# Performance work log

Measured on AMD Instinct MI355X. Metric: run time of the kernel, lower is better.

The kernel has to match this reference:

```python
import jax, jax.numpy as jnp
import numpy as np

INPUT_DIM = 28
OUTPUT_DIM = 21
LAYER_SIZE = 64
NUM_HIDDEN = 10  # number of 64x64 hidden layers after the input layer


def setup_inputs() -> dict:
    key = jax.random.key(0)
    ks = jax.random.split(key, 7)
    x = jax.random.normal(ks[0], (1048576, INPUT_DIM), dtype=jnp.float32)
    # PyTorch nn.Linear default init: U(-1/sqrt(fan_in), 1/sqrt(fan_in)); plain uniform is fine for a baseline.
    s_in = 1.0 / np.sqrt(INPUT_DIM)
    s_h = 1.0 / np.sqrt(LAYER_SIZE)
    W_in = jax.random.uniform(ks[1], (INPUT_DIM, LAYER_SIZE), jnp.float32, -s_in, s_in)
    b_in = jax.random.uniform(ks[2], (LAYER_SIZE,), jnp.float32, -s_in, s_in)
    W_hid = jax.random.uniform(ks[3], (NUM_HIDDEN, LAYER_SIZE, LAYER_SIZE), jnp.float32, -s_h, s_h)
    b_hid = jax.random.uniform(ks[4], (NUM_HIDDEN, LAYER_SIZE), jnp.float32, -s_h, s_h)
    W_out = jax.random.uniform(ks[5], (LAYER_SIZE, OUTPUT_DIM), jnp.float32, -s_h, s_h)
    b_out = jax.random.uniform(ks[6], (OUTPUT_DIM,), jnp.float32, -s_h, s_h)
    return {"x": x, "W_in": W_in, "b_in": b_in, "W_hid": W_hid, "b_hid": b_hid,
            "W_out": W_out, "b_out": b_out}


def reference(x, W_in, b_in, W_hid, b_hid, W_out, b_out):
    h = jax.nn.relu(x @ W_in + b_in)  # [B, 64]
    def step(h, wb):
        W, b = wb
        return jax.nn.relu(h @ W + b), None
    h, _ = jax.lax.scan(step, h, (W_hid, b_hid))
    return jax.nn.sigmoid(h @ W_out + b_out)  # [B, 21]
```

## Files before the change

### kernel.cpp

```cpp
#include <hip/hip_runtime.h>

#define DEV __device__ __forceinline__
#define SBAR() __builtin_amdgcn_sched_barrier(0)

typedef _Float16 half8 __attribute__((ext_vector_type(8)));
typedef _Float16 half2v __attribute__((ext_vector_type(2)));
typedef float f32x16 __attribute__((ext_vector_type(16)));
typedef int int4v __attribute__((ext_vector_type(4)));

DEV f32x16 mfma16(half8 a, half8 b, f32x16 c) {
    return __builtin_amdgcn_mfma_f32_32x32x16_f16(a, b, c, 0, 0, 0);
}
DEV half8 h8(int4v v) { return __builtin_bit_cast(half8, v); }
DEV half8 ldh8(const _Float16* p) { return *(const half8*)p; }
DEV int pkrtz(float a, float b) {
    auto t = __builtin_amdgcn_cvt_pkrtz(a, b);
    return __builtin_bit_cast(int, t);
}
DEV int relupk(float a, float b) {
    int p = pkrtz(a, b);
    half2v h = __builtin_bit_cast(half2v, p);
    half2v z = {(_Float16)0.f, (_Float16)0.f};
    h = __builtin_elementwise_max(h, z);
    return __builtin_bit_cast(int, h);
}
DEV void plswap(int& a, int& b) {
    asm("v_permlane32_swap_b32 %0, %1" : "+v"(a), "+v"(b));
}

DEV f32x16 zero16() {
    f32x16 z = {0.f,0.f,0.f,0.f,0.f,0.f,0.f,0.f,0.f,0.f,0.f,0.f,0.f,0.f,0.f,0.f};
    return z;
}

struct Frags { int4v c[4]; };

DEV void repack(const f32x16& C0, const f32x16& C1, Frags& B) {
    int P0[8], P1[8];
#pragma unroll
    for (int q = 0; q < 8; ++q) {
        P0[q] = relupk(C0[2*q], C0[2*q+1]);
        P1[q] = relupk(C1[2*q], C1[2*q+1]);
    }
#pragma unroll
    for (int kk = 0; kk < 4; ++kk) {
        const int* Pm = (kk < 2) ? P0 : P1;
        int idx = 4 * (kk & 1);
        int a0 = Pm[idx + 0], b0 = Pm[idx + 2];
        int a1 = Pm[idx + 1], b1 = Pm[idx + 3];
        plswap(a0, b0);
        plswap(a1, b1);
        int4v nb; nb[0] = a0; nb[1] = a1; nb[2] = b0; nb[3] = b1;
        B.c[kk] = nb;
    }
}

DEV void loadA5(const _Float16* base, int lam, half8* A0, half8* A1) {
    const _Float16* p0 = base + lam * 8;
    const _Float16* p1 = base + 2560 + lam * 8;
#pragma unroll
    for (int kk = 0; kk < 5; ++kk) {
        A0[kk] = ldh8(p0 + kk * 512);
        A1[kk] = ldh8(p1 + kk * 512);
    }
}

DEV void mfma_hid_t(const half8* A0, const half8* A1, half8 ones, const Frags& Bx,
                    f32x16& C0, f32x16& C1) {
    C0 = mfma16(A0[4], ones, zero16());
    C1 = mfma16(A1[4], ones, zero16());
#pragma unroll
    for (int kk = 0; kk < 4; ++kk) {
        half8 b = h8(Bx.c[kk]);
        C0 = mfma16(A0[kk], b, C0);
        C1 = mfma16(A1[kk], b, C1);
    }
}

DEV void mfma_in_t(const half8* I, const Frags& Bx, f32x16& C0, f32x16& C1) {
    C0 = mfma16(I[0], h8(Bx.c[0]), zero16());
    C1 = mfma16(I[2], h8(Bx.c[0]), zero16());
    C0 = mfma16(I[1], h8(Bx.c[1]), C0);
    C1 = mfma16(I[3], h8(Bx.c[1]), C1);
}

DEV void mfma_out_t(const half8* Ao, half8 ones, const Frags& Bx, f32x16& C) {
    C = mfma16(Ao[4], ones, zero16());
#pragma unroll
    for (int kk = 0; kk < 4; ++kk) C = mfma16(Ao[kk], h8(Bx.c[kk]), C);
}

DEV void store_out(const f32x16& C, int h, float* __restrict__ out, int row) {
    float* o = out + row * 21;
#pragma unroll
    for (int r = 0; r < 16; ++r) {
        int f = (r & 3) + 8 * (r >> 2) + 4 * h;
        if (f < 21) o[f] = __builtin_amdgcn_rcpf(1.f + __expf(-C[r]));
    }
}

DEV void load_x(const float* __restrict__ x, int row, int h, Frags& B) {
    const float* xr = x + row * 28;
    float4 fa = *(const float4*)(xr + 8 * h);
    float4 fb = *(const float4*)(xr + 8 * h + 4);
    float4 fc = *(const float4*)(xr + 16 + 8 * h);
    float4 fd = (h == 0) ? *(const float4*)(xr + 20) : make_float4(1.f, 0.f, 0.f, 0.f);
    int4v c0, c1;
    c0[0] = pkrtz(fa.x, fa.y); c0[1] = pkrtz(fa.z, fa.w);
    c0[2] = pkrtz(fb.x, fb.y); c0[3] = pkrtz(fb.z, fb.w);
    c1[0] = pkrtz(fc.x, fc.y); c1[1] = pkrtz(fc.z, fc.w);
    c1[2] = pkrtz(fd.x, fd.y); c1[3] = pkrtz(fd.z, fd.w);
    B.c[0] = c0; B.c[1] = c1;
}

#define NT 512

__global__ __attribute__((amdgpu_flat_work_group_size(NT, NT), amdgpu_waves_per_eu(2, 2)))
void mlp_fused(
    const float* __restrict__ x, const float* __restrict__ W_in, const float* __restrict__ b_in,
    const float* __restrict__ W_hid, const float* __restrict__ b_hid,
    const float* __restrict__ W_out, const float* __restrict__ b_out,
    float* __restrict__ out) {
    __shared__ __align__(16) _Float16 wH[51200];
    __shared__ __align__(16) _Float16 wI[2048];
    __shared__ __align__(16) _Float16 wO[2560];

    const int tid = threadIdx.x;

    for (int i = tid; i < 10240; i += NT) {
        int l = i >> 10, rem = i & 1023, m = rem >> 9, off = rem & 511;
        wH[l * 5120 + m * 2560 + 2048 + off] = (_Float16)0.f;
    }
    for (int i = tid; i < 2048; i += NT) wI[i] = (_Float16)0.f;
    for (int i = tid; i < 2560; i += NT) wO[i] = (_Float16)0.f;
    __syncthreads();

    for (int i = tid; i < 40960; i += NT) {
        int o = i & 63, kin = (i >> 6) & 63, l = i >> 12;
        int m = o >> 5, kk = kin >> 4, hh = (kin >> 3) & 1, e = kin & 7;
        int lam = hh * 32 + (o & 31);
        wH[l * 5120 + m * 2560 + kk * 512 + lam * 8 + e] = (_Float16)W_hid[i];
    }
    for (int i = tid; i < 640; i += NT) {
        int l = i >> 6, f = i & 63, m = f >> 5, r = f & 31;
        wH[l * 5120 + m * 2560 + 2048 + r * 8] = (_Float16)b_hid[i];
    }
    for (int i = tid; i < 1792; i += NT) {
        int o = i & 63, kin = i >> 6;
        int m = o >> 5, kk = kin >> 4, hh = (kin >> 3) & 1, e = kin & 7;
        int lam = hh * 32 + (o & 31);
        wI[m * 1024 + kk * 512 + lam * 8 + e] = (_Float16)W_in[i];
    }
    for (int i = tid; i < 64; i += NT) {
        int m = i >> 5;
        wI[m * 1024 + 512 + (32 + (i & 31)) * 8 + 4] = (_Float16)b_in[i];
    }
    for (int i = tid; i < 1344; i += NT) {
        int o = i % 21, kin = i / 21;
        int kk = kin >> 4, hh = (kin >> 3) & 1, e = kin & 7;
        int lam = hh * 32 + o;
        wO[kk * 512 + lam * 8 + e] = (_Float16)W_out[i];
    }
    for (int i = tid; i < 21; i += NT)
        wO[4 * 512 + i * 8] = (_Float16)b_out[i];
    __syncthreads();

    const int w = tid >> 6, lam = tid & 63;
    const int col = lam & 31, h = lam >> 5;
    int4v onesv; onesv[0] = (h == 0) ? 0x3C00 : 0; onesv[1] = 0; onesv[2] = 0; onesv[3] = 0;
    half8 ones = h8(onesv);

    half8 I[4], Ao[5];
    {
        const _Float16* p0 = wI + lam * 8;
        const _Float16* p1 = wI + 1024 + lam * 8;
        I[0] = ldh8(p0);       I[1] = ldh8(p0 + 512);
        I[2] = ldh8(p1);       I[3] = ldh8(p1 + 512);
        const _Float16* po = wO + lam * 8;
#pragma unroll
        for (int kk = 0; kk < 5; ++kk) Ao[kk] = ldh8(po + kk * 512);
    }

    const int tbase = blockIdx.x * 128;
#pragma unroll 1
    for (int j = 0; j < 8; ++j) {
        int tA = tbase + w * 16 + 2 * j;
        int rowA = tA * 32 + col, rowB = rowA + 32;
        Frags BA, BB;
        load_x(x, rowA, h, BA);
        load_x(x, rowB, h, BB);

        half8 Fa0[5], Fa1[5], Fb0[5], Fb1[5];
        f32x16 CA0, CA1, CB0, CB1;

        mfma_in_t(I, BA, CA0, CA1);
        loadA5(wH, lam, Fa0, Fa1);
        mfma_in_t(I, BB, CB0, CB1);
        repack(CA0, CA1, BA);
        SBAR();

#pragma unroll
        for (int l2 = 0; l2 < 5; ++l2) {
            const _Float16* b0 = wH + (2 * l2) * 5120;
            mfma_hid_t(Fa0, Fa1, ones, BA, CA0, CA1);
            loadA5(b0 + 5120, lam, Fb0, Fb1);
            repack(CB0, CB1, BB);
            SBAR();
            mfma_hid_t(Fa0, Fa1, ones, BB, CB0, CB1);
            repack(CA0, CA1, BA);
            SBAR();
            mfma_hid_t(Fb0, Fb1, ones, BA, CA0, CA1);
            if (l2 < 4) loadA5(b0 + 10240, lam, Fa0, Fa1);
            repack(CB0, CB1, BB);
            SBAR();
            mfma_hid_t(Fb0, Fb1, ones, BB, CB0, CB1);
            repack(CA0, CA1, BA);
            SBAR();
        }

        f32x16 CoA, CoB;
        mfma_out_t(Ao, ones, BA, CoA);
        repack(CB0, CB1, BB);
        SBAR();
        mfma_out_t(Ao, ones, BB, CoB);
        store_out(CoA, h, out, rowA);
        store_out(CoB, h, out, rowB);
    }
}

extern "C" void kernel_launch(void* const* d_in, const int* in_sizes, int n_in,
                              void* d_out, int out_size, void* d_ws, size_t ws_size,
                              hipStream_t stream) {
    const float* x     = (const float*)d_in[0];
    const float* W_in  = (const float*)d_in[1];
    const float* b_in  = (const float*)d_in[2];
    const float* W_hid = (const float*)d_in[3];
    const float* b_hid = (const float*)d_in[4];
    const float* W_out = (const float*)d_in[5];
    const float* b_out = (const float*)d_in[6];
    float* out = (float*)d_out;
    mlp_fused<<<dim3(256), dim3(NT), 0, stream>>>(x, W_in, b_in, W_hid, b_hid, W_out, b_out, out);
}
```

Baseline: 105.9 us.

## Batch both row tiles' MFMAs per layer and raise priority around MFMA bursts

Replaces the staggered ping-pong schedule, in which tile A's MFMAs overlapped tile B's repack, with a schedule that runs both tiles' MFMAs back-to-back for each layer and then repacks both. Interleaving independent A and B accumulators gives the matrix unit more independent chains. It also wraps each MFMA burst in s_setprio so this wave's matrix work gets issue priority over the other waves' VALU repack phases. The cost is that the intra-wave overlap of repack with MFMA is lost, and the design relies on cross-wave overlap, with two waves per EU, to hide the repack instead.

After: 102.2 us. -3.5%, faster.

```diff
diff --git a/kernel.cpp b/kernel.cpp
--- a/kernel.cpp
+++ b/kernel.cpp
@@ -65,29 +65,45 @@
     }
 }
 
-DEV void mfma_hid_t(const half8* A0, const half8* A1, half8 ones, const Frags& Bx,
-                    f32x16& C0, f32x16& C1) {
-    C0 = mfma16(A0[4], ones, zero16());
-    C1 = mfma16(A1[4], ones, zero16());
+DEV void mfma_hid_AB(const half8* A0, const half8* A1, half8 ones,
+                     const Frags& BA, const Frags& BB,
+                     f32x16& CA0, f32x16& CA1, f32x16& CB0, f32x16& CB1) {
+    CA0 = mfma16(A0[4], ones, zero16());
+    CB0 = mfma16(A0[4], ones, zero16());
+    CA1 = mfma16(A1[4], ones, zero16());
+    CB1 = mfma16(A1[4], ones, zero16());
 #pragma unroll
     for (int kk = 0; kk < 4; ++kk) {
-        half8 b = h8(Bx.c[kk]);
-        C0 = mfma16(A0[kk], b, C0);
-        C1 = mfma16(A1[kk], b, C1);
-    }
-}
-
-DEV void mfma_in_t(const half8* I, const Frags& Bx, f32x16& C0, f32x16& C1) {
-    C0 = mfma16(I[0], h8(Bx.c[0]), zero16());
-    C1 = mfma16(I[2], h8(Bx.c[0]), zero16());
-    C0 = mfma16(I[1], h8(Bx.c[1]), C0);
-    C1 = mfma16(I[3], h8(Bx.c[1]), C1);
-}
-
-DEV void mfma_out_t(const half8* Ao, half8 ones, const Frags& Bx, f32x16& C) {
-    C = mfma16(Ao[4], ones, zero16());
-#pragma unroll
-    for (int kk = 0; kk < 4; ++kk) C = mfma16(Ao[kk], h8(Bx.c[kk]), C);
+        half8 bA = h8(BA.c[kk]);
+        half8 bB = h8(BB.c[kk]);
+        CA0 = mfma16(A0[kk], bA, CA0);
+        CB0 = mfma16(A0[kk], bB, CB0);
+        CA1 = mfma16(A1[kk], bA, CA1);
+        CB1 = mfma16(A1[kk], bB, CB1);
+    }
+}
+
+DEV void mfma_in_AB(const half8* I, const Frags& BA, const Frags& BB,
+                    f32x16& CA0, f32x16& CA1, f32x16& CB0, f32x16& CB1) {
+    CA0 = mfma16(I[0], h8(BA.c[0]), zero16());
+    CB0 = mfma16(I[0], h8(BB.c[0]), zero16());
+    CA1 = mfma16(I[2], h8(BA.c[0]), zero16());
+    CB1 = mfma16(I[2], h8(BB.c[0]), zero16());
+    CA0 = mfma16(I[1], h8(BA.c[1]), CA0);
+    CB0 = mfma16(I[1], h8(BB.c[1]), CB0);
+    CA1 = mfma16(I[3], h8(BA.c[1]), CA1);
+    CB1 = mfma16(I[3], h8(BB.c[1]), CB1);
+}
+
+DEV void mfma_out_AB(const half8* Ao, half8 ones, const Frags& BA, const Frags& BB,
+                     f32x16& CoA, f32x16& CoB) {
+    CoA = mfma16(Ao[4], ones, zero16());
+    CoB = mfma16(Ao[4], ones, zero16());
+#pragma unroll
+    for (int kk = 0; kk < 4; ++kk) {
+        CoA = mfma16(Ao[kk], h8(BA.c[kk]), CoA);
+        CoB = mfma16(Ao[kk], h8(BB.c[kk]), CoB);
+    }
 }
 
 DEV void store_out(const f32x16& C, int h, float* __restrict__ out, int row) {
@@ -193,36 +209,37 @@
         half8 Fa0[5], Fa1[5], Fb0[5], Fb1[5];
         f32x16 CA0, CA1, CB0, CB1;
 
-        mfma_in_t(I, BA, CA0, CA1);
+        __builtin_amdgcn_s_setprio(1);
+        mfma_in_AB(I, BA, BB, CA0, CA1, CB0, CB1);
+        __builtin_amdgcn_s_setprio(0);
         loadA5(wH, lam, Fa0, Fa1);
-        mfma_in_t(I, BB, CB0, CB1);
         repack(CA0, CA1, BA);
+        repack(CB0, CB1, BB);
         SBAR();
 
 #pragma unroll
         for (int l2 = 0; l2 < 5; ++l2) {
             const _Float16* b0 = wH + (2 * l2) * 5120;
-            mfma_hid_t(Fa0, Fa1, ones, BA, CA0, CA1);
+            __builtin_amdgcn_s_setprio(1);
+            mfma_hid_AB(Fa0, Fa1, ones, BA, BB, CA0, CA1, CB0, CB1);
+            __builtin_amdgcn_s_setprio(0);
             loadA5(b0 + 5120, lam, Fb0, Fb1);
+            repack(CA0, CA1, BA);
             repack(CB0, CB1, BB);
             SBAR();
-            mfma_hid_t(Fa0, Fa1, ones, BB, CB0, CB1);
+            __builtin_amdgcn_s_setprio(1);
+            mfma_hid_AB(Fb0, Fb1, ones, BA, BB, CA0, CA1, CB0, CB1);
+            __builtin_amdgcn_s_setprio(0);
+            if (l2 < 4) loadA5(b0 + 10240, lam, Fa0, Fa1);
             repack(CA0, CA1, BA);
-            SBAR();
-            mfma_hid_t(Fb0, Fb1, ones, BA, CA0, CA1);
-            if (l2 < 4) loadA5(b0 + 10240, lam, Fa0, Fa1);
             repack(CB0, CB1, BB);
             SBAR();
-            mfma_hid_t(Fb0, Fb1, ones, BB, CB0, CB1);
-            repack(CA0, CA1, BA);
-            SBAR();
         }
 
         f32x16 CoA, CoB;
-        mfma_out_t(Ao, ones, BA, CoA);
-        repack(CB0, CB1, BB);
-        SBAR();
-        mfma_out_t(Ao, ones, BB, CoB);
+        __builtin_amdgcn_s_setprio(1);
+        mfma_out_AB(Ao, ones, BA, BB, CoA, CoB);
+        __builtin_amdgcn_s_setprio(0);
         store_out(CoA, h, out, rowA);
         store_out(CoB, h, out, rowB);
     }
```

## Permute weight K-layout to drop permlane swaps in activation repack

Applied to the files above, without the earlier changes.

Rearranges the K ordering of hidden and output weights in shared memory so the MFMA accumulator layout maps directly onto the next layer's B-operand fragments. This removes the v_permlane32_swap instructions from repack, leaving only relu+pack conversions. It also removes the explicit sched_barrier calls, giving the compiler freedom to interleave repack with MFMAs. The input-layer weights keep the old layout, which is fine only if the K permutation is consistent between the producing and consuming layers. Scheduling freedom may or may not reproduce the hand-tuned interleave.

New measurement: 271.4 us. 156% more time.

```diff
diff --git a/kernel.cpp b/kernel.cpp
--- a/kernel.cpp
+++ b/kernel.cpp
@@ -1,7 +1,6 @@
 #include <hip/hip_runtime.h>
 
 #define DEV __device__ __forceinline__
-#define SBAR() __builtin_amdgcn_sched_barrier(0)
 
 typedef _Float16 half8 __attribute__((ext_vector_type(8)));
 typedef _Float16 half2v __attribute__((ext_vector_type(2)));
@@ -24,9 +23,6 @@
     h = __builtin_elementwise_max(h, z);
     return __builtin_bit_cast(int, h);
 }
-DEV void plswap(int& a, int& b) {
-    asm("v_permlane32_swap_b32 %0, %1" : "+v"(a), "+v"(b));
-}
 
 DEV f32x16 zero16() {
     f32x16 z = {0.f,0.f,0.f,0.f,0.f,0.f,0.f,0.f,0.f,0.f,0.f,0.f,0.f,0.f,0.f,0.f};
@@ -36,23 +32,15 @@
 struct Frags { int4v c[4]; };
 
 DEV void repack(const f32x16& C0, const f32x16& C1, Frags& B) {
-    int P0[8], P1[8];
-#pragma unroll
-    for (int q = 0; q < 8; ++q) {
-        P0[q] = relupk(C0[2*q], C0[2*q+1]);
-        P1[q] = relupk(C1[2*q], C1[2*q+1]);
-    }
-#pragma unroll
-    for (int kk = 0; kk < 4; ++kk) {
-        const int* Pm = (kk < 2) ? P0 : P1;
-        int idx = 4 * (kk & 1);
-        int a0 = Pm[idx + 0], b0 = Pm[idx + 2];
-        int a1 = Pm[idx + 1], b1 = Pm[idx + 3];
-        plswap(a0, b0);
-        plswap(a1, b1);
-        int4v nb; nb[0] = a0; nb[1] = a1; nb[2] = b0; nb[3] = b1;
-        B.c[kk] = nb;
-    }
+    int4v b0, b1, b2, b3;
+#pragma unroll
+    for (int q = 0; q < 4; ++q) {
+        b0[q] = relupk(C0[2*q],     C0[2*q+1]);
+        b1[q] = relupk(C0[8+2*q],   C0[9+2*q]);
+        b2[q] = relupk(C1[2*q],     C1[2*q+1]);
+        b3[q] = relupk(C1[8+2*q],   C1[9+2*q]);
+    }
+    B.c[0] = b0; B.c[1] = b1; B.c[2] = b2; B.c[3] = b3;
 }
 
 DEV void loadA5(const _Float16* base, int lam, half8* A0, half8* A1) {
@@ -137,7 +125,9 @@
 
     for (int i = tid; i < 40960; i += NT) {
         int o = i & 63, kin = (i >> 6) & 63, l = i >> 12;
-        int m = o >> 5, kk = kin >> 4, hh = (kin >> 3) & 1, e = kin & 7;
+        int m = o >> 5, kk = kin >> 4;
+        int hh = (kin >> 2) & 1;
+        int e = (kin & 3) + 4 * ((kin >> 3) & 1);
         int lam = hh * 32 + (o & 31);
         wH[l * 5120 + m * 2560 + kk * 512 + lam * 8 + e] = (_Float16)W_hid[i];
     }
@@ -157,7 +147,9 @@
     }
     for (int i = tid; i < 1344; i += NT) {
         int o = i % 21, kin = i / 21;
-        int kk = kin >> 4, hh = (kin >> 3) & 1, e = kin & 7;
+        int kk = kin >> 4;
+        int hh = (kin >> 2) & 1;
+        int e = (kin & 3) + 4 * ((kin >> 3) & 1);
         int lam = hh * 32 + o;
         wO[kk * 512 + lam * 8 + e] = (_Float16)W_out[i];
     }
@@ -197,7 +189,6 @@
         loadA5(wH, lam, Fa0, Fa1);
         mfma_in_t(I, BB, CB0, CB1);
         repack(CA0, CA1, BA);
-        SBAR();
 
 #pragma unroll
         for (int l2 = 0; l2 < 5; ++l2) {
@@ -205,23 +196,18 @@
             mfma_hid_t(Fa0, Fa1, ones, BA, CA0, CA1);
             loadA5(b0 + 5120, lam, Fb0, Fb1);
             repack(CB0, CB1, BB);
-            SBAR();
             mfma_hid_t(Fa0, Fa1, ones, BB, CB0, CB1);
             repack(CA0, CA1, BA);
-            SBAR();
             mfma_hid_t(Fb0, Fb1, ones, BA, CA0, CA1);
             if (l2 < 4) loadA5(b0 + 10240, lam, Fa0, Fa1);
             repack(CB0, CB1, BB);
-            SBAR();
             mfma_hid_t(Fb0, Fb1, ones, BB, CB0, CB1);
             repack(CA0, CA1, BA);
-            SBAR();
         }
 
         f32x16 CoA, CoB;
         mfma_out_t(Ao, ones, BA, CoA);
         repack(CB0, CB1, BB);
-        SBAR();
         mfma_out_t(Ao, ones, BB, CoB);
         store_out(CoA, h, out, rowA);
         store_out(CoB, h, out, rowB);
```
